# Kernel tuning notes

Hardware: AMD Instinct MI355X
Metric: run time of the kernel (lower is better)

The kernel has to match this reference:

```python
import jax, jax.numpy as jnp
import numpy as np

NEG_SLOPE = 0.2


def gat_conv(x, edge_index, W, a_src, a_dst, b, concat):
    """PyG-style GATConv: add self-loops, linear, edge attention, scatter-softmax, scatter-add."""
    N = x.shape[0]
    H, C = a_src.shape
    loop = jnp.arange(N)
    src = jnp.concatenate([edge_index[0], loop])  # source j (messages flow j -> i)
    dst = jnp.concatenate([edge_index[1], loop])  # target i (aggregation node)
    h = (x @ W).reshape(N, H, C)                  # [N,H,C]
    alpha_s = jnp.sum(h * a_src, axis=-1)         # [N,H]
    alpha_d = jnp.sum(h * a_dst, axis=-1)         # [N,H]
    e = jax.nn.leaky_relu(alpha_s[src] + alpha_d[dst], NEG_SLOPE)  # [E,H]
    # numerically stable scatter-softmax over edges grouped by destination node
    m = jax.ops.segment_max(e, dst, num_segments=N)                # [N,H]
    ex = jnp.exp(e - m[dst])
    denom = jax.ops.segment_sum(ex, dst, num_segments=N)           # [N,H]
    alpha = ex / (denom[dst] + 1e-16)                              # [E,H]
    out = jax.ops.segment_sum(h[src] * alpha[:, :, None], dst, num_segments=N)  # [N,H,C]
    out = out.reshape(N, H * C) if concat else out.mean(axis=1)
    return out + b


def setup_inputs() -> dict:
    key = jax.random.key(0)
    ks = jax.random.split(key, 12)
    N, E, F_IN, HID, OUT, HEADS = 100000, 1600000, 128, 128, 64, 4
    C1 = HID // HEADS
    x = jax.random.normal(ks[0], (N, F_IN), dtype=jnp.float32)
    edge_index = jax.random.randint(ks[1], (2, E), 0, N, dtype=jnp.int64)
    s = 0.05
    return {
        "x": x,
        "edge_index": edge_index,
        "W1": jax.random.normal(ks[2], (F_IN, HEADS * C1), dtype=jnp.float32) * s,
        "a_src1": jax.random.normal(ks[3], (HEADS, C1), dtype=jnp.float32) * s,
        "a_dst1": jax.random.normal(ks[4], (HEADS, C1), dtype=jnp.float32) * s,
        "b1": jnp.zeros((HEADS * C1,), dtype=jnp.float32),
        "W2": jax.random.normal(ks[5], (HID, OUT), dtype=jnp.float32) * s,
        "a_src2": jax.random.normal(ks[6], (1, OUT), dtype=jnp.float32) * s,
        "a_dst2": jax.random.normal(ks[7], (1, OUT), dtype=jnp.float32) * s,
        "b2": jnp.zeros((OUT,), dtype=jnp.float32),
    }


def reference(x, edge_index, W1, a_src1, a_dst1, b1, W2, a_src2, a_dst2, b2):
    h = jax.nn.elu(gat_conv(x, edge_index, W1, a_src1, a_dst1, b1, concat=True))
    # F.dropout(p=0.5, training=False) is the identity in eval mode
    out = gat_conv(h, edge_index, W2, a_src2, a_dst2, b2, concat=False)
    return out
```

## Files before the change

kernel.cpp:

```cpp
#include <hip/hip_runtime.h>
#include <hip/hip_fp16.h>
#include <math.h>
#include <string.h>


#define BSH 9
#define DPB 512
#define NBK 256
#define CH1 16384
#define LOG2E 1.44269504088896f

using half8 = __attribute__((ext_vector_type(8))) _Float16;
using floatx4 = __attribute__((ext_vector_type(4))) float;

__device__ __forceinline__ float exp2_fast(float x) {
#if __has_builtin(__builtin_amdgcn_exp2f)
    return __builtin_amdgcn_exp2f(x);
#else
    return exp2f(x);
#endif
}


__global__ __launch_bounds__(256) void bucket_hist(const int* __restrict__ ei, int E, int N,
                                                   unsigned* __restrict__ bcount) {
    __shared__ unsigned hist[NBK];
    int t = threadIdx.x;
    hist[t] = 0;
    __syncthreads();
    int Etot = E + N;
    for (int k = blockIdx.x * 256 + t; k < Etot; k += gridDim.x * 256) {
        int d = (k < E) ? ei[E + k] : (k - E);
        atomicAdd(&hist[d >> BSH], 1u);
    }
    __syncthreads();
    unsigned c = hist[t];
    if (c) atomicAdd(&bcount[t], c);
}

__global__ void scan_buckets(const unsigned* __restrict__ bcount, unsigned* __restrict__ bbase,
                             unsigned* __restrict__ bcursor) {
    __shared__ unsigned s[NBK];
    int t = threadIdx.x;
    unsigned v = bcount[t];
    s[t] = v;
    __syncthreads();
    for (int o = 1; o < NBK; o <<= 1) {
        unsigned add = (t >= o) ? s[t - o] : 0;
        __syncthreads();
        s[t] += add;
        __syncthreads();
    }
    unsigned excl = s[t] - v;
    bbase[t] = excl;
    bcursor[t] = excl;
    if (t == NBK - 1) bbase[NBK] = excl + v;
}

__global__ __launch_bounds__(256) void bucket_scatter(const int* __restrict__ ei, int E, int N,
                                                      unsigned* __restrict__ bcursor,
                                                      unsigned* __restrict__ rec) {
    __shared__ unsigned hist[NBK];
    __shared__ unsigned base[NBK];
    int t = threadIdx.x;
    hist[t] = 0;
    __syncthreads();
    int Etot = E + N;
    int k0 = blockIdx.x * CH1;
    int k1 = min(k0 + CH1, Etot);
    for (int k = k0 + t; k < k1; k += 256) {
        int d = (k < E) ? ei[E + k] : (k - E);
        atomicAdd(&hist[d >> BSH], 1u);
    }
    __syncthreads();
    unsigned c = hist[t];
    base[t] = c ? atomicAdd(&bcursor[t], c) : 0u;
    hist[t] = 0;
    __syncthreads();
    for (int k = k0 + t; k < k1; k += 256) {
        int s, d;
        if (k < E) { s = ei[k]; d = ei[E + k]; } else { s = d = k - E; }
        int b = d >> BSH;
        unsigned r = atomicAdd(&hist[b], 1u);
        rec[base[b] + r] = (unsigned)s | ((unsigned)(d & (DPB - 1)) << 17);
    }
}

__global__ __launch_bounds__(256) void bucket_sort(const unsigned* __restrict__ rec,
                                                   const unsigned* __restrict__ bbase,
                                                   int* __restrict__ offs, int* __restrict__ srcs,
                                                   int N, int Etot) {
    __shared__ unsigned hist[DPB];
    __shared__ unsigned tsum[256];
    int t = threadIdx.x, bb = blockIdx.x;
    unsigned r0 = bbase[bb], r1 = bbase[bb + 1];
    hist[t] = 0;
    hist[t + 256] = 0;
    __syncthreads();
    int dlo = bb << BSH;
    for (unsigned k = r0 + t; k < r1; k += 256) {
        unsigned e = rec[k];
        atomicAdd(&hist[e >> 17], 1u);
    }
    __syncthreads();
    unsigned h0 = hist[2 * t], h1 = hist[2 * t + 1];
    tsum[t] = h0 + h1;
    __syncthreads();
    for (int o = 1; o < 256; o <<= 1) {
        unsigned a = (t >= o) ? tsum[t - o] : 0;
        __syncthreads();
        tsum[t] += a;
        __syncthreads();
    }
    unsigned tb = tsum[t] - (h0 + h1);
    int d0 = dlo + 2 * t;
    if (d0 < N) offs[d0] = (int)(r0 + tb);
    if (d0 + 1 < N) offs[d0 + 1] = (int)(r0 + tb + h0);
    hist[2 * t] = tb;
    hist[2 * t + 1] = tb + h0;
    __syncthreads();
    for (unsigned k = r0 + t; k < r1; k += 256) {
        unsigned e = rec[k];
        unsigned r = atomicAdd(&hist[e >> 17], 1u);
        srcs[r0 + r] = (int)(e & 0x1FFFFu);
    }
    if (bb == 0 && t == 0) offs[N] = Etot;
}


__global__ void transpose_w(const float* __restrict__ W, __half* __restrict__ Wt,
                            int K, int Nc) {
    int idx = blockIdx.x * 256 + threadIdx.x;
    if (idx >= K * Nc) return;
    int n = idx / K, k = idx - n * K;
    Wt[n * K + k] = __float2half(W[k * Nc + n]);
}


template <int NC, int H, typename InT>
__global__ __launch_bounds__(256) void gemm_mfma(const InT* __restrict__ A,
                                                 const __half* __restrict__ Wt,
                                                 __half* __restrict__ C,
                                                 const float* __restrict__ a_src,
                                                 const float* __restrict__ a_dst,
                                                 float* __restrict__ as,
                                                 float* __restrict__ ad, int M) {
    constexpr int NT = NC / 16;
    constexpr int TPH = NT / H;
    int wave = threadIdx.x >> 6;
    int lane = threadIdx.x & 63;
    int quad = lane >> 4, col = lane & 15;
    int row0 = blockIdx.x * 64 + wave * 16;
    int arow = row0 + col;
    if (arow >= M) arow = M - 1;
    floatx4 acc[NT] = {};
    const __half* wp = Wt + col * 128 + quad * 8;
#pragma unroll
    for (int k0 = 0; k0 < 128; k0 += 32) {
        half8 af;
        if constexpr (sizeof(InT) == 4) {
            const float* ap = (const float*)A + (size_t)arow * 128 + k0 + quad * 8;
            float4 v0 = *reinterpret_cast<const float4*>(ap);
            float4 v1 = *reinterpret_cast<const float4*>(ap + 4);
            af[0] = (_Float16)v0.x; af[1] = (_Float16)v0.y;
            af[2] = (_Float16)v0.z; af[3] = (_Float16)v0.w;
            af[4] = (_Float16)v1.x; af[5] = (_Float16)v1.y;
            af[6] = (_Float16)v1.z; af[7] = (_Float16)v1.w;
        } else {
            af = *reinterpret_cast<const half8*>((const __half*)A + (size_t)arow * 128 + k0 + quad * 8);
        }
#pragma unroll
        for (int t = 0; t < NT; ++t) {
            half8 bf = *reinterpret_cast<const half8*>(wp + t * 16 * 128 + k0);
            acc[t] = __builtin_amdgcn_mfma_f32_16x16x32_f16(af, bf, acc[t], 0, 0, 0);
        }
    }
    float sa[NT], da[NT];
#pragma unroll
    for (int t = 0; t < NT; ++t) {
        sa[t] = a_src[t * 16 + col];
        da[t] = a_dst[t * 16 + col];
    }
    int rbase = row0 + quad * 4;
#pragma unroll
    for (int reg = 0; reg < 4; ++reg) {
        int row = rbase + reg;
        bool live = row < M;
        if (live) {
#pragma unroll
            for (int t = 0; t < NT; ++t)
                C[(size_t)row * NC + t * 16 + col] = __float2half(acc[t][reg]);
        }
#pragma unroll
        for (int h = 0; h < H; ++h) {
            float ps = 0.f, pd = 0.f;
#pragma unroll
            for (int tt = 0; tt < TPH; ++tt) {
                int t = h * TPH + tt;
                ps = fmaf(acc[t][reg], sa[t], ps);
                pd = fmaf(acc[t][reg], da[t], pd);
            }
#pragma unroll
            for (int o = 1; o < 16; o <<= 1) {
                ps += __shfl_xor(ps, o, 64);
                pd += __shfl_xor(pd, o, 64);
            }
            if (col == 0 && live) {
                as[(size_t)row * H + h] = ps * LOG2E;
                ad[(size_t)row * H + h] = pd * LOG2E;
            }
        }
    }
}


template <int H, int ROWS, int CW, bool DOELU, typename OutT>
__global__ __launch_bounds__(256) void aggregateQ(const __half* __restrict__ h,
                                                  const float* __restrict__ as,
                                                  const float* __restrict__ ad,
                                                  const int* __restrict__ offs,
                                                  const int* __restrict__ srcs,
                                                  const float* __restrict__ bias,
                                                  OutT* __restrict__ out, int N) {
    constexpr int CPL = CW / 16;
    constexpr int NH2 = CPL / 2;
    unsigned wave = (blockIdx.x * blockDim.x + threadIdx.x) >> 6;
    unsigned lane = threadIdx.x & 63;
    unsigned lig = lane & 15;
    unsigned node = wave * 4u + (lane >> 4);
    bool live = node < (unsigned)N;
    unsigned nc = live ? node : (unsigned)(N - 1);
    unsigned chan = lig * CPL;
    unsigned head = (chan * H) / ROWS;
    float adv = ad[nc * H + head];
    int e0 = offs[nc], e1 = offs[nc + 1];
    int deg = e1 - e0, e1m1 = e1 - 1;
    int md = deg;
    md = max(md, __shfl_xor(md, 16, 64));
    md = max(md, __shfl_xor(md, 32, 64));
    float2 acc[NH2] = {};
    float den = 0.f;
    for (int k = 0; k < md; k += 2) {
        unsigned ja = (unsigned)srcs[min(e0 + k, e1m1)];
        unsigned jb = (unsigned)srcs[min(e0 + k + 1, e1m1)];
        float ta = as[ja * H + head] + adv;
        float tb = as[jb * H + head] + adv;
        __half2 ha[NH2], hb[NH2];
        if constexpr (NH2 == 4) {
            uint4 va = *reinterpret_cast<const uint4*>(h + ja * (unsigned)ROWS + chan);
            uint4 vb = *reinterpret_cast<const uint4*>(h + jb * (unsigned)ROWS + chan);
            memcpy(ha, &va, 16);
            memcpy(hb, &vb, 16);
        } else {
            uint2 va = *reinterpret_cast<const uint2*>(h + ja * (unsigned)ROWS + chan);
            uint2 vb = *reinterpret_cast<const uint2*>(h + jb * (unsigned)ROWS + chan);
            memcpy(ha, &va, 8);
            memcpy(hb, &vb, 8);
        }
        float xa = exp2_fast(fmaxf(ta, 0.2f * ta));
        float xb = exp2_fast(fmaxf(tb, 0.2f * tb));
        xa = (k < deg) ? xa : 0.f;
        xb = (k + 1 < deg) ? xb : 0.f;
#pragma unroll
        for (int q = 0; q < NH2; ++q) {
            float2 fa = __half22float2(ha[q]);
            float2 fb = __half22float2(hb[q]);
            acc[q].x = fmaf(xa, fa.x, acc[q].x);
            acc[q].y = fmaf(xa, fa.y, acc[q].y);
            acc[q].x = fmaf(xb, fb.x, acc[q].x);
            acc[q].y = fmaf(xb, fb.y, acc[q].y);
        }
        den += xa + xb;
    }
    float r = 1.0f / (den + 1e-16f);
    if (!live) return;
    const float* bp = bias + chan;
    if constexpr (sizeof(OutT) == 2) {
        __half2 st[NH2];
#pragma unroll
        for (int q = 0; q < NH2; ++q) {
            float v0 = acc[q].x * r + bp[2 * q];
            float v1 = acc[q].y * r + bp[2 * q + 1];
            if constexpr (DOELU) {
                v0 = (v0 > 0.f) ? v0 : expm1f(v0);
                v1 = (v1 > 0.f) ? v1 : expm1f(v1);
            }
            st[q] = __floats2half2_rn(v0, v1);
        }
        if constexpr (NH2 == 4) {
            uint4 v; memcpy(&v, st, 16);
            *reinterpret_cast<uint4*>((__half*)out + node * (unsigned)ROWS + chan) = v;
        } else {
            uint2 v; memcpy(&v, st, 8);
            *reinterpret_cast<uint2*>((__half*)out + node * (unsigned)ROWS + chan) = v;
        }
    } else {
        float vs[CPL];
#pragma unroll
        for (int q = 0; q < NH2; ++q) {
            float v0 = acc[q].x * r + bp[2 * q];
            float v1 = acc[q].y * r + bp[2 * q + 1];
            if constexpr (DOELU) {
                v0 = (v0 > 0.f) ? v0 : expm1f(v0);
                v1 = (v1 > 0.f) ? v1 : expm1f(v1);
            }
            vs[2 * q] = v0;
            vs[2 * q + 1] = v1;
        }
#pragma unroll
        for (int q4 = 0; q4 < CPL; q4 += 4) {
            float4 v = make_float4(vs[q4], vs[q4 + 1], vs[q4 + 2], vs[q4 + 3]);
            *reinterpret_cast<float4*>((float*)out + node * (unsigned)ROWS + chan + q4) = v;
        }
    }
}


extern "C" void kernel_launch(void* const* d_in, const int* in_sizes, int n_in,
                              void* d_out, int out_size, void* d_ws, size_t ws_size,
                              hipStream_t stream) {
    const float* x      = (const float*)d_in[0];
    const int*   ei     = (const int*)d_in[1];
    const float* W1     = (const float*)d_in[2];
    const float* a_src1 = (const float*)d_in[3];
    const float* a_dst1 = (const float*)d_in[4];
    const float* b1     = (const float*)d_in[5];
    const float* W2     = (const float*)d_in[6];
    const float* a_src2 = (const float*)d_in[7];
    const float* a_dst2 = (const float*)d_in[8];
    const float* b2     = (const float*)d_in[9];
    float* out = (float*)d_out;

    const int N = out_size / 64;
    const int E = in_sizes[1] / 2;
    const int Etot = E + N;

    size_t off = 0;
    auto carve = [&](size_t bytes) -> void* {
        void* p = (char*)d_ws + off;
        off += (bytes + 255) & ~(size_t)255;
        return p;
    };
    __half* h1      = (__half*)carve((size_t)N * 128 * 2);
    __half* hmid    = (__half*)carve((size_t)N * 128 * 2);
    float* as1      = (float*)carve((size_t)N * 4 * 4);
    float* ad1      = (float*)carve((size_t)N * 4 * 4);
    float* as2      = (float*)carve((size_t)N * 4);
    float* ad2      = (float*)carve((size_t)N * 4);
    int*   offs     = (int*)carve((size_t)(N + 1) * 4);
    int*   srcs     = (int*)carve((size_t)Etot * 4);
    unsigned* rec   = (unsigned*)carve((size_t)Etot * 4);
    unsigned* bcount  = (unsigned*)carve(NBK * 4);
    unsigned* bbase   = (unsigned*)carve((NBK + 1) * 4);
    unsigned* bcursor = (unsigned*)carve(NBK * 4);
    __half* Wt1h    = (__half*)carve(128 * 128 * 2);
    __half* Wt2h    = (__half*)carve(64 * 128 * 2);
    __half* h2      = h1;

    hipMemsetAsync(bcount, 0, NBK * sizeof(unsigned), stream);
    bucket_hist<<<128, 256, 0, stream>>>(ei, E, N, bcount);
    scan_buckets<<<1, 256, 0, stream>>>(bcount, bbase, bcursor);
    bucket_scatter<<<(Etot + CH1 - 1) / CH1, 256, 0, stream>>>(ei, E, N, bcursor, rec);
    bucket_sort<<<(N + DPB - 1) / DPB, 256, 0, stream>>>(rec, bbase, offs, srcs, N, Etot);

    transpose_w<<<64, 256, 0, stream>>>(W1, Wt1h, 128, 128);
    transpose_w<<<32, 256, 0, stream>>>(W2, Wt2h, 128, 64);

    gemm_mfma<128, 4, float><<<(N + 63) / 64, 256, 0, stream>>>(
        x, Wt1h, h1, a_src1, a_dst1, as1, ad1, N);
    aggregateQ<4, 128, 128, true, __half><<<(N + 15) / 16, 256, 0, stream>>>(
        h1, as1, ad1, offs, srcs, b1, hmid, N);

    gemm_mfma<64, 1, __half><<<(N + 63) / 64, 256, 0, stream>>>(
        hmid, Wt2h, h2, a_src2, a_dst2, as2, ad2, N);
    aggregateQ<1, 64, 64, false, float><<<(N + 15) / 16, 256, 0, stream>>>(
        h2, as2, ad2, offs, srcs, b2, out, N);
}
```

Baseline: 379.2 us.

## Process aggregation nodes in descending-degree order to balance wave workloads

Builds a degree histogram while sorting edges, scans it, and counting-sorts node ids into an order array. Both aggregation kernels then map nodes from this order in descending degree, so the four nodes sharing a wave have similar degrees and less time is lost to the max-degree loop bound. It also merges the two weight-transpose launches into one. The cost is two extra small kernels, scattered output writes and a loss of locality when reading per-node data.

```diff
diff --git a/kernel.cpp b/kernel.cpp
--- a/kernel.cpp
+++ b/kernel.cpp
@@ -8,6 +8,8 @@
 #define DPB 512
 #define NBK 256
 #define CH1 16384
+#define DBINS 512
+#define OCH 1024
 #define LOG2E 1.44269504088896f
 
 using half8 = __attribute__((ext_vector_type(8))) _Float16;
@@ -89,13 +91,17 @@
 __global__ __launch_bounds__(256) void bucket_sort(const unsigned* __restrict__ rec,
                                                    const unsigned* __restrict__ bbase,
                                                    int* __restrict__ offs, int* __restrict__ srcs,
+                                                   unsigned* __restrict__ deghist,
                                                    int N, int Etot) {
     __shared__ unsigned hist[DPB];
     __shared__ unsigned tsum[256];
+    __shared__ unsigned deg_l[DBINS];
     int t = threadIdx.x, bb = blockIdx.x;
     unsigned r0 = bbase[bb], r1 = bbase[bb + 1];
     hist[t] = 0;
     hist[t + 256] = 0;
+    deg_l[t] = 0;
+    deg_l[t + 256] = 0;
     __syncthreads();
     int dlo = bb << BSH;
     for (unsigned k = r0 + t; k < r1; k += 256) {
@@ -104,6 +110,9 @@
     }
     __syncthreads();
     unsigned h0 = hist[2 * t], h1 = hist[2 * t + 1];
+    int d0 = dlo + 2 * t;
+    if (d0 < N) atomicAdd(&deg_l[min(h0, (unsigned)(DBINS - 1))], 1u);
+    if (d0 + 1 < N) atomicAdd(&deg_l[min(h1, (unsigned)(DBINS - 1))], 1u);
     tsum[t] = h0 + h1;
     __syncthreads();
     for (int o = 1; o < 256; o <<= 1) {
@@ -113,7 +122,6 @@
         __syncthreads();
     }
     unsigned tb = tsum[t] - (h0 + h1);
-    int d0 = dlo + 2 * t;
     if (d0 < N) offs[d0] = (int)(r0 + tb);
     if (d0 + 1 < N) offs[d0 + 1] = (int)(r0 + tb + h0);
     hist[2 * t] = tb;
@@ -125,15 +133,70 @@
         srcs[r0 + r] = (int)(e & 0x1FFFFu);
     }
     if (bb == 0 && t == 0) offs[N] = Etot;
-}
-
-
-__global__ void transpose_w(const float* __restrict__ W, __half* __restrict__ Wt,
-                            int K, int Nc) {
+    unsigned c0 = deg_l[t], c1 = deg_l[t + 256];
+    if (c0) atomicAdd(&deghist[t], c0);
+    if (c1) atomicAdd(&deghist[t + 256], c1);
+}
+
+
+__global__ void scan_deg(const unsigned* __restrict__ deghist, unsigned* __restrict__ degcur) {
+    __shared__ unsigned s[DBINS];
+    int t = threadIdx.x;
+    unsigned v = deghist[t];
+    s[t] = v;
+    __syncthreads();
+    for (int o = 1; o < DBINS; o <<= 1) {
+        unsigned a = (t >= o) ? s[t - o] : 0;
+        __syncthreads();
+        s[t] += a;
+        __syncthreads();
+    }
+    degcur[t] = s[t] - v;
+}
+
+__global__ __launch_bounds__(256) void order_scatter(const int* __restrict__ offs,
+                                                     unsigned* __restrict__ degcur,
+                                                     int* __restrict__ order, int N) {
+    __shared__ unsigned hist[DBINS];
+    __shared__ unsigned base[DBINS];
+    int t = threadIdx.x;
+    hist[t] = 0;
+    hist[t + 256] = 0;
+    __syncthreads();
+    int k0 = blockIdx.x * OCH, k1 = min(k0 + OCH, N);
+    for (int k = k0 + t; k < k1; k += 256) {
+        int deg = offs[k + 1] - offs[k];
+        atomicAdd(&hist[min(deg, DBINS - 1)], 1u);
+    }
+    __syncthreads();
+    for (int i = t; i < DBINS; i += 256) {
+        unsigned c = hist[i];
+        base[i] = c ? atomicAdd(&degcur[i], c) : 0u;
+        hist[i] = 0;
+    }
+    __syncthreads();
+    for (int k = k0 + t; k < k1; k += 256) {
+        int deg = offs[k + 1] - offs[k];
+        int b = min(deg, DBINS - 1);
+        unsigned r = atomicAdd(&hist[b], 1u);
+        order[base[b] + r] = k;
+    }
+}
+
+
+__global__ void transpose_both(const float* __restrict__ W1, const float* __restrict__ W2,
+                               __half* __restrict__ Wt1, __half* __restrict__ Wt2) {
     int idx = blockIdx.x * 256 + threadIdx.x;
-    if (idx >= K * Nc) return;
-    int n = idx / K, k = idx - n * K;
-    Wt[n * K + k] = __float2half(W[k * Nc + n]);
+    if (idx < 128 * 128) {
+        int n = idx >> 7, k = idx & 127;
+        Wt1[idx] = __float2half(W1[k * 128 + n]);
+    } else {
+        int j = idx - 128 * 128;
+        if (j < 64 * 128) {
+            int n = j >> 7, k = j & 127;
+            Wt2[j] = __float2half(W2[k * 64 + n]);
+        }
+    }
 }
 
 
@@ -220,6 +283,7 @@
                                                   const float* __restrict__ ad,
                                                   const int* __restrict__ offs,
                                                   const int* __restrict__ srcs,
+                                                  const int* __restrict__ order,
                                                   const float* __restrict__ bias,
                                                   OutT* __restrict__ out, int N) {
     constexpr int CPL = CW / 16;
@@ -227,9 +291,9 @@
     unsigned wave = (blockIdx.x * blockDim.x + threadIdx.x) >> 6;
     unsigned lane = threadIdx.x & 63;
     unsigned lig = lane & 15;
-    unsigned node = wave * 4u + (lane >> 4);
-    bool live = node < (unsigned)N;
-    unsigned nc = live ? node : (unsigned)(N - 1);
+    unsigned idx = wave * 4u + (lane >> 4);
+    bool live = idx < (unsigned)N;
+    unsigned nc = (unsigned)order[live ? ((unsigned)N - 1u - idx) : 0u];
     unsigned chan = lig * CPL;
     unsigned head = (chan * H) / ROWS;
     float adv = ad[nc * H + head];
@@ -289,10 +353,10 @@
         }
         if constexpr (NH2 == 4) {
             uint4 v; memcpy(&v, st, 16);
-            *reinterpret_cast<uint4*>((__half*)out + node * (unsigned)ROWS + chan) = v;
+            *reinterpret_cast<uint4*>((__half*)out + nc * (unsigned)ROWS + chan) = v;
         } else {
             uint2 v; memcpy(&v, st, 8);
-            *reinterpret_cast<uint2*>((__half*)out + node * (unsigned)ROWS + chan) = v;
+            *reinterpret_cast<uint2*>((__half*)out + nc * (unsigned)ROWS + chan) = v;
         }
     } else {
         float vs[CPL];
@@ -310,7 +374,7 @@
 #pragma unroll
         for (int q4 = 0; q4 < CPL; q4 += 4) {
             float4 v = make_float4(vs[q4], vs[q4 + 1], vs[q4 + 2], vs[q4 + 3]);
-            *reinterpret_cast<float4*>((float*)out + node * (unsigned)ROWS + chan + q4) = v;
+            *reinterpret_cast<float4*>((float*)out + nc * (unsigned)ROWS + chan + q4) = v;
         }
     }
 }
@@ -350,29 +414,35 @@
     int*   offs     = (int*)carve((size_t)(N + 1) * 4);
     int*   srcs     = (int*)carve((size_t)Etot * 4);
     unsigned* rec   = (unsigned*)carve((size_t)Etot * 4);
-    unsigned* bcount  = (unsigned*)carve(NBK * 4);
+    unsigned* ctrs  = (unsigned*)carve((NBK + DBINS) * 4);
     unsigned* bbase   = (unsigned*)carve((NBK + 1) * 4);
     unsigned* bcursor = (unsigned*)carve(NBK * 4);
+    unsigned* degcur  = (unsigned*)carve(DBINS * 4);
     __half* Wt1h    = (__half*)carve(128 * 128 * 2);
     __half* Wt2h    = (__half*)carve(64 * 128 * 2);
+    unsigned* bcount  = ctrs;
+    unsigned* deghist = ctrs + NBK;
+    int* order      = (int*)rec;
     __half* h2      = h1;
 
-    hipMemsetAsync(bcount, 0, NBK * sizeof(unsigned), stream);
+    hipMemsetAsync(ctrs, 0, (NBK + DBINS) * sizeof(unsigned), stream);
     bucket_hist<<<128, 256, 0, stream>>>(ei, E, N, bcount);
     scan_buckets<<<1, 256, 0, stream>>>(bcount, bbase, bcursor);
     bucket_scatter<<<(Etot + CH1 - 1) / CH1, 256, 0, stream>>>(ei, E, N, bcursor, rec);
-    bucket_sort<<<(N + DPB - 1) / DPB, 256, 0, stream>>>(rec, bbase, offs, srcs, N, Etot);
-
-    transpose_w<<<64, 256, 0, stream>>>(W1, Wt1h, 128, 128);
-    transpose_w<<<32, 256, 0, stream>>>(W2, Wt2h, 128, 64);
+    bucket_sort<<<(N + DPB - 1) / DPB, 256, 0, stream>>>(rec, bbase, offs, srcs, deghist, N, Etot);
+
+    scan_deg<<<1, DBINS, 0, stream>>>(deghist, degcur);
+    order_scatter<<<(N + OCH - 1) / OCH, 256, 0, stream>>>(offs, degcur, order, N);
+
+    transpose_both<<<96, 256, 0, stream>>>(W1, W2, Wt1h, Wt2h);
 
     gemm_mfma<128, 4, float><<<(N + 63) / 64, 256, 0, stream>>>(
         x, Wt1h, h1, a_src1, a_dst1, as1, ad1, N);
     aggregateQ<4, 128, 128, true, __half><<<(N + 15) / 16, 256, 0, stream>>>(
-        h1, as1, ad1, offs, srcs, b1, hmid, N);
+        h1, as1, ad1, offs, srcs, order, b1, hmid, N);
 
     gemm_mfma<64, 1, __half><<<(N + 63) / 64, 256, 0, stream>>>(
         hmid, Wt2h, h2, a_src2, a_dst2, as2, ad2, N);
     aggregateQ<1, 64, 64, false, float><<<(N + 15) / 16, 256, 0, stream>>>(
-        h2, as2, ad2, offs, srcs, b2, out, N);
-}
+        h2, as2, ad2, offs, srcs, order, b2, out, N);
+}
```

Result: no change. 379.2 us (-0.0%).
